# Performance work log

Measured on AMD Instinct MI355X. Metric: run time of the kernel, lower is better.

The kernel has to match this reference:

```python
import jax, jax.numpy as jnp
import numpy as np

B, S, K, N = 4, 2048, 1024, 4096


def setup_inputs() -> dict:
    key = jax.random.key(0)
    k1, k2, k3, k4, k5 = jax.random.split(key, 5)
    # int8 activations/weights as produced by static affine quantization (zero_point_domain=NONE)
    x_int8 = jax.random.randint(k1, (B, S, K), -128, 128, dtype=jnp.int32).astype(jnp.int8)
    w_int8 = jax.random.randint(k2, (N, K), -128, 128, dtype=jnp.int32).astype(jnp.int8)
    scale_i = jax.random.uniform(k3, (), minval=0.01, maxval=0.05, dtype=jnp.float32)   # per-tensor act scale
    scale_w = jax.random.uniform(k4, (N,), minval=0.001, maxval=0.01, dtype=jnp.float32)  # per-channel weight scale
    bias = jax.random.normal(k5, (N,), dtype=jnp.float32)
    return {"x_int8": x_int8, "w_int8": w_int8, "scale_i": scale_i, "scale_w": scale_w, "bias": bias}


def q(x, dtype):
    # denormal-flushing cast from the source; for float32 it is a plain cast
    # (module.weight.dtype == float32 here), kept as a helper for fidelity.
    if dtype == jnp.float16:
        return jnp.where(jnp.abs(x) < 2.0 ** -14, jnp.zeros_like(x), x).astype(jnp.float16)
    if dtype == jnp.bfloat16:
        return jnp.where(jnp.abs(x) < 2.0 ** -126, jnp.zeros_like(x), x).astype(jnp.bfloat16)
    return x.astype(dtype)


def reference(x_int8, w_int8, scale_i, scale_w, bias):
    # 'quantized'-mode forward of QModule wrapping a Linear:
    #   x = q(round(F.linear(x.double(), w.double())), dtype) * q(q(scale_i*scale_w, f32), f32)
    #   x = x + bias
    # round(double matmul of int8 values) is exact integer accumulation, so an
    # int32 GEMM is bit-identical (|acc| <= 127*127*1024 << 2^53 and < 2^31).
    acc = jnp.einsum('bsk,nk->bsn', x_int8.astype(jnp.int32), w_int8.astype(jnp.int32))  # [B,S,N] int32
    scale = q(q(scale_i * scale_w, jnp.float32), jnp.float32)  # [N]
    out = q(acc, jnp.float32) * scale + bias  # fused dequant/rescale + bias epilogue
    return out
```

## Files before the change

### kernel.cpp

```cpp
#include <hip/hip_runtime.h>
#include <stdint.h>

#define M_DIM 8192
#define N_DIM 4096
#define K_DIM 1024
#define BK    128

using i32x4  = __attribute__((ext_vector_type(4))) int;
using i32x16 = __attribute__((ext_vector_type(16))) int;

__global__ __launch_bounds__(256) void pack_both(const int* __restrict__ X32,
                                                 const int* __restrict__ W32,
                                                 int* __restrict__ Xp,
                                                 int* __restrict__ Wp) {
    int b = blockIdx.x;
    const int4* s4;
    int4* d4;
    int u;
    if (b < 2048) {
        u  = b * 256 + threadIdx.x;
        s4 = (const int4*)X32;
        d4 = (int4*)Xp;
    } else {
        u  = (b - 2048) * 256 + threadIdx.x;
        s4 = (const int4*)W32;
        d4 = (int4*)Wp;
    }
    int4 o;
    #pragma unroll
    for (int i = 0; i < 4; ++i) {
        int4 v = s4[u * 4 + i];
        ((int*)&o)[i] = (v.x & 0xFF) | ((v.y & 0xFF) << 8) |
                        ((v.z & 0xFF) << 16) | (v.w << 24);
    }
    d4[u] = o;
}

__device__ __forceinline__ void cp16_async(const void* g, void* l) {
    __builtin_amdgcn_global_load_lds(
        (const __attribute__((address_space(1))) void*)g,
        (__attribute__((address_space(3))) void*)l,
        16, 0, 0);
}

__global__ __launch_bounds__(256, 3) void i8gemm_dequant(
    const int8_t* __restrict__ X,
    const int8_t* __restrict__ W,
    const float*  __restrict__ scale_i,
    const float*  __restrict__ scale_w,
    const float*  __restrict__ bias,
    float*        __restrict__ out)
{
    __shared__ int8_t lA[128 * BK];
    __shared__ int8_t lB[128 * BK];

    const int t     = threadIdx.x;
    const int lane  = t & 63;
    const int wave  = t >> 6;
    const int waveM = wave >> 1;
    const int waveN = wave & 1;

    const int bm = blockIdx.y * 128;
    const int bn = blockIdx.x * 128;

    i32x16 acc[2][2] = {};

    const int8_t* Asrc[4];
    const int8_t* Bsrc[4];
    int8_t* dA[4];
    int8_t* dB[4];
    #pragma unroll
    for (int s = 0; s < 4; ++s) {
        int c   = t + 256 * s;
        int row = c >> 3;
        int q   = (c & 7) ^ (row & 7);
        Asrc[s] = X + (size_t)(bm + row) * K_DIM + q * 16;
        Bsrc[s] = W + (size_t)(bn + row) * K_DIM + q * 16;
        dA[s]   = lA + (256 * s + wave * 64) * 16;
        dB[s]   = lB + (256 * s + wave * 64) * 16;
    }

    int aoff[4][2], boff[4][2];
    #pragma unroll
    for (int s = 0; s < 4; ++s) {
        #pragma unroll
        for (int i = 0; i < 2; ++i) {
            int r = waveM * 64 + i * 32 + (lane & 31);
            int q = (s * 2 + (lane >> 5)) ^ (r & 7);
            aoff[s][i] = r * BK + q * 16;
        }
        #pragma unroll
        for (int j = 0; j < 2; ++j) {
            int r = waveN * 64 + j * 32 + (lane & 31);
            int q = (s * 2 + (lane >> 5)) ^ (r & 7);
            boff[s][j] = r * BK + q * 16;
        }
    }

    for (int k0 = 0; k0 < K_DIM; k0 += BK) {
        #pragma unroll
        for (int s = 0; s < 4; ++s) {
            cp16_async(Asrc[s] + k0, dA[s]);
            cp16_async(Bsrc[s] + k0, dB[s]);
        }
        __syncthreads();

        i32x4 af[4][2], bf[4][2];
        #pragma unroll
        for (int s = 0; s < 4; ++s) {
            #pragma unroll
            for (int i = 0; i < 2; ++i) af[s][i] = *(const i32x4*)(lA + aoff[s][i]);
            #pragma unroll
            for (int j = 0; j < 2; ++j) bf[s][j] = *(const i32x4*)(lB + boff[s][j]);
        }

        #pragma unroll
        for (int s = 0; s < 4; ++s)
            #pragma unroll
            for (int i = 0; i < 2; ++i)
                #pragma unroll
                for (int j = 0; j < 2; ++j)
                    acc[i][j] = __builtin_amdgcn_mfma_i32_32x32x32_i8(
                        af[s][i], bf[s][j], acc[i][j], 0, 0, 0);

        __syncthreads();
    }

    const float si = scale_i[0];
    float s[2], b[2];
    int   ncol[2];
    #pragma unroll
    for (int j = 0; j < 2; ++j) {
        ncol[j] = bn + waveN * 64 + j * 32 + (lane & 31);
        s[j] = si * scale_w[ncol[j]];
        b[j] = bias[ncol[j]];
    }
    const int rbase = 4 * (lane >> 5);
    #pragma unroll
    for (int i = 0; i < 2; ++i) {
        int mbase = bm + waveM * 64 + i * 32 + rbase;
        #pragma unroll
        for (int reg = 0; reg < 16; ++reg) {
            int m = mbase + (reg & 3) + 8 * (reg >> 2);
            size_t rowoff = (size_t)m * N_DIM;
            #pragma unroll
            for (int j = 0; j < 2; ++j) {
                out[rowoff + ncol[j]] = (float)acc[i][j][reg] * s[j] + b[j];
            }
        }
    }
}

extern "C" void kernel_launch(void* const* d_in, const int* in_sizes, int n_in,
                              void* d_out, int out_size, void* d_ws, size_t ws_size,
                              hipStream_t stream) {
    const int* x32 = (const int*)d_in[0];
    const int* w32 = (const int*)d_in[1];
    const float* si = (const float*)d_in[2];
    const float* sw = (const float*)d_in[3];
    const float* bs = (const float*)d_in[4];
    float* out = (float*)d_out;

    int8_t* Xp = (int8_t*)d_ws;
    int8_t* Wp = (int8_t*)d_ws + (size_t)M_DIM * K_DIM;

    pack_both<<<3072, 256, 0, stream>>>(x32, w32, (int*)Xp, (int*)Wp);

    dim3 grid(N_DIM / 128, M_DIM / 128);
    i8gemm_dequant<<<grid, 256, 0, stream>>>(Xp, Wp, si, sw, bs, out);
}
```

Measured before the change: 201.0 us.

## Double-buffer LDS tiles with BK=64 to overlap global loads with MFMA

```diff
diff --git a/kernel.cpp b/kernel.cpp
--- a/kernel.cpp
+++ b/kernel.cpp
@@ -4,7 +4,7 @@
 #define M_DIM 8192
 #define N_DIM 4096
 #define K_DIM 1024
-#define BK    128
+#define BK    64
 
 using i32x4  = __attribute__((ext_vector_type(4))) int;
 using i32x16 = __attribute__((ext_vector_type(16))) int;
@@ -51,8 +51,8 @@
     const float*  __restrict__ bias,
     float*        __restrict__ out)
 {
-    __shared__ int8_t lA[128 * BK];
-    __shared__ int8_t lB[128 * BK];
+    __shared__ int8_t lA[2][128 * BK];
+    __shared__ int8_t lB[2][128 * BK];
 
     const int t     = threadIdx.x;
     const int lane  = t & 63;
@@ -65,65 +65,73 @@
 
     i32x16 acc[2][2] = {};
 
-    const int8_t* Asrc[4];
-    const int8_t* Bsrc[4];
-    int8_t* dA[4];
-    int8_t* dB[4];
+    const int8_t* Asrc[2];
+    const int8_t* Bsrc[2];
+    int ldso[2];
     #pragma unroll
-    for (int s = 0; s < 4; ++s) {
+    for (int s = 0; s < 2; ++s) {
         int c   = t + 256 * s;
-        int row = c >> 3;
-        int q   = (c & 7) ^ (row & 7);
+        int row = c >> 2;
+        int q   = (c & 3) ^ ((row >> 1) & 3);
         Asrc[s] = X + (size_t)(bm + row) * K_DIM + q * 16;
         Bsrc[s] = W + (size_t)(bn + row) * K_DIM + q * 16;
-        dA[s]   = lA + (256 * s + wave * 64) * 16;
-        dB[s]   = lB + (256 * s + wave * 64) * 16;
+        ldso[s] = (256 * s + wave * 64) * 16;
     }
 
-    int aoff[4][2], boff[4][2];
+    int aoff[2][2], boff[2][2];
     #pragma unroll
-    for (int s = 0; s < 4; ++s) {
+    for (int s = 0; s < 2; ++s) {
         #pragma unroll
         for (int i = 0; i < 2; ++i) {
             int r = waveM * 64 + i * 32 + (lane & 31);
-            int q = (s * 2 + (lane >> 5)) ^ (r & 7);
+            int q = (s * 2 + (lane >> 5)) ^ ((r >> 1) & 3);
             aoff[s][i] = r * BK + q * 16;
         }
         #pragma unroll
         for (int j = 0; j < 2; ++j) {
             int r = waveN * 64 + j * 32 + (lane & 31);
-            int q = (s * 2 + (lane >> 5)) ^ (r & 7);
+            int q = (s * 2 + (lane >> 5)) ^ ((r >> 1) & 3);
             boff[s][j] = r * BK + q * 16;
         }
     }
 
-    for (int k0 = 0; k0 < K_DIM; k0 += BK) {
-        #pragma unroll
-        for (int s = 0; s < 4; ++s) {
-            cp16_async(Asrc[s] + k0, dA[s]);
-            cp16_async(Bsrc[s] + k0, dB[s]);
-        }
+    #pragma unroll
+    for (int s = 0; s < 2; ++s) {
+        cp16_async(Asrc[s], &lA[0][ldso[s]]);
+        cp16_async(Bsrc[s], &lB[0][ldso[s]]);
+    }
+
+    #pragma unroll 2
+    for (int it = 0; it < 16; ++it) {
+        const int cur = it & 1;
         __syncthreads();
 
-        i32x4 af[4][2], bf[4][2];
+        if (it < 15) {
+            int knext = (it + 1) * BK;
+            #pragma unroll
+            for (int s = 0; s < 2; ++s) {
+                cp16_async(Asrc[s] + knext, &lA[cur ^ 1][ldso[s]]);
+                cp16_async(Bsrc[s] + knext, &lB[cur ^ 1][ldso[s]]);
+            }
+        }
+
+        i32x4 af[2][2], bf[2][2];
         #pragma unroll
-        for (int s = 0; s < 4; ++s) {
+        for (int s = 0; s < 2; ++s) {
             #pragma unroll
-            for (int i = 0; i < 2; ++i) af[s][i] = *(const i32x4*)(lA + aoff[s][i]);
+            for (int i = 0; i < 2; ++i) af[s][i] = *(const i32x4*)(&lA[cur][0] + aoff[s][i]);
             #pragma unroll
-            for (int j = 0; j < 2; ++j) bf[s][j] = *(const i32x4*)(lB + boff[s][j]);
+            for (int j = 0; j < 2; ++j) bf[s][j] = *(const i32x4*)(&lB[cur][0] + boff[s][j]);
         }
 
         #pragma unroll
-        for (int s = 0; s < 4; ++s)
+        for (int s = 0; s < 2; ++s)
             #pragma unroll
             for (int i = 0; i < 2; ++i)
                 #pragma unroll
                 for (int j = 0; j < 2; ++j)
                     acc[i][j] = __builtin_amdgcn_mfma_i32_32x32x32_i8(
                         af[s][i], bf[s][j], acc[i][j], 0, 0, 0);
-
-        __syncthreads();
     }
 
     const float si = scale_i[0];
```

After: 206.2 us. 2.6% more time.
